# Kernel optimization log

Measured on AMD Instinct MI355X. Metric: run time of the kernel, lower is better.

The kernel has to match this reference:

```python
import jax, jax.numpy as jnp
import numpy as np

N_NODES = 50000
N_EDGES = 800000
IN_DIM = 256
OUT_DIM = 64
HEADS = 8


def setup_inputs() -> dict:
    key = jax.random.key(0)
    k1, k2, k3, k4, k5 = jax.random.split(key, 5)
    x = jax.random.normal(k1, (N_NODES, IN_DIM), dtype=jnp.float32)
    edge_index = jax.random.randint(k2, (2, N_EDGES), 0, N_NODES, dtype=jnp.int32)
    W = jax.random.normal(k3, (HEADS, IN_DIM, OUT_DIM), dtype=jnp.float32) / np.sqrt(IN_DIM)
    b = jnp.zeros((HEADS, OUT_DIM), dtype=jnp.float32)
    a = jax.random.normal(k4, (HEADS, 2 * OUT_DIM), dtype=jnp.float32)
    gate = jnp.ones((HEADS,), dtype=jnp.float32)
    return {"x": x, "edge_index": edge_index, "W": W, "b": b, "a": a, "gate": gate}


def reference(x, edge_index, W, b, a, gate):
    # Wh: [H, N, O] -- per-head linear projections
    Wh = jnp.einsum('nd,hdo->hno', x, W) + b[:, None, :]
    row, col = edge_index[0], edge_index[1]
    O = Wh.shape[-1]
    a_src, a_dst = a[:, :O], a[:, O:]  # split of concat weight: [H, O] each
    # score per edge per head: leaky_relu(cat(Wh[row], Wh[col]) @ a)
    e = (jnp.einsum('heo,ho->he', Wh[:, row], a_src)
         + jnp.einsum('heo,ho->he', Wh[:, col], a_dst))  # [H, E]
    e = jax.nn.leaky_relu(e, negative_slope=0.01)
    # NOTE: original code softmaxes over ALL edges (dim=0), not per node
    alpha = jax.nn.softmax(e, axis=1)  # [H, E]
    msgs = alpha[:, :, None] * Wh[:, col, :]  # [H, E, O]
    out = jax.vmap(lambda m: jax.ops.segment_sum(m, row, num_segments=Wh.shape[1]))(msgs)  # [H, N, O]
    g = jax.nn.softmax(gate)
    return jnp.einsum('h,hno->no', g, out)
```

## Files before the change

### kernel.cpp

```cpp
#include <hip/hip_runtime.h>
#include <hip/hip_bf16.h>


#define N_NODES 50000
#define N_EDGES 800000
#define IN_DIM  256
#define OUT_DIM 64
#define HEADS   8
#define NCOL    (HEADS * OUT_DIM)
#define NBLK_RED 2048
#define LN_W_EPS (-20.72326584f)

typedef __attribute__((ext_vector_type(8))) short short8;
typedef __attribute__((ext_vector_type(4))) float f32x4;

__device__ __forceinline__ void bf16_split2(float x0, float x1,
                                            unsigned& hi, unsigned& lo)
{
    unsigned u0 = __float_as_uint(x0), u1 = __float_as_uint(x1);
    unsigned r0 = u0 + 0x7FFFu + ((u0 >> 16) & 1u);
    unsigned r1 = u1 + 0x7FFFu + ((u1 >> 16) & 1u);
    float h0 = __uint_as_float(r0 & 0xFFFF0000u);
    float h1 = __uint_as_float(r1 & 0xFFFF0000u);
    hi = (r0 >> 16) | (r1 & 0xFFFF0000u);
    unsigned l0 = __float_as_uint(x0 - h0);
    unsigned l1 = __float_as_uint(x1 - h1);
    lo = (l0 >> 16) | (l1 & 0xFFFF0000u);
}

__global__ __launch_bounds__(256) void packw_kernel(
    const float* __restrict__ W, short* __restrict__ wp)
{
    const int ct = blockIdx.x;
    const int h  = ct >> 2;
    #pragma unroll
    for (int it = 0; it < 2; ++it) {
        const int i  = threadIdx.x + it * 256;
        const int k8 = i >> 4;
        const int c  = i & 15;
        const int o  = (ct & 3) * 16 + c;
        const float* src = W + (size_t)h * IN_DIM * OUT_DIM
                             + (size_t)k8 * 8 * OUT_DIM + o;
        unsigned hi[4], lo[4];
        #pragma unroll
        for (int p = 0; p < 4; ++p) {
            float x0 = src[(2 * p) * OUT_DIM];
            float x1 = src[(2 * p + 1) * OUT_DIM];
            bf16_split2(x0, x1, hi[p], lo[p]);
        }
        uint4 vh = make_uint4(hi[0], hi[1], hi[2], hi[3]);
        uint4 vl = make_uint4(lo[0], lo[1], lo[2], lo[3]);
        *(uint4*)(wp + (((size_t)(ct * 2 + 0) * 32 + k8) * 128) + c * 8) = vh;
        *(uint4*)(wp + (((size_t)(ct * 2 + 1) * 32 + k8) * 128) + c * 8) = vl;
    }
}

__global__ __launch_bounds__(512, 2) void gemm_kernel(
    const float* __restrict__ x, const short* __restrict__ wp,
    const float* __restrict__ b, const float* __restrict__ a,
    float* __restrict__ s_src, float* __restrict__ s_dst)
{
    __shared__ __align__(16) short As[32768];
    __shared__ __align__(16) float s_tmp[2][64][8];

    const int row0 = blockIdx.x * 64;
    const int tid  = threadIdx.x;
    const int lane = tid & 63;
    const int head = tid >> 6;
    const int r16  = lane & 15;
    const int kq   = lane >> 4;

    const short* pB = wp + (size_t)kq * 128 + (size_t)r16 * 8;
    #define LD_B(ni, s, ks) \
        (*(const short8*)(pB + ((((size_t)(head * 4 + (ni)) * 2 + (s)) * 32 + 4 * (ks)) * 128)))
    short8 Bh[2][4], Bl[2][4];
    #pragma unroll
    for (int ni = 0; ni < 4; ++ni) { Bh[0][ni] = LD_B(ni, 0, 0); Bl[0][ni] = LD_B(ni, 1, 0); }

    f32x4 vv[4][2];
    #pragma unroll
    for (int q = 0; q < 4; ++q) {
        const int item = q * 512 + tid;
        const int row  = item >> 5;
        const int kc   = item & 31;
        const int grow = row0 + row;
        vv[q][0] = (f32x4){0.f, 0.f, 0.f, 0.f};
        vv[q][1] = (f32x4){0.f, 0.f, 0.f, 0.f};
        if (grow < N_NODES) {
            vv[q][0] = *(const f32x4*)(x + (size_t)grow * IN_DIM + kc * 8);
            vv[q][1] = *(const f32x4*)(x + (size_t)grow * IN_DIM + kc * 8 + 4);
        }
    }
    __builtin_amdgcn_sched_barrier(0);

    #pragma unroll
    for (int q = 0; q < 4; ++q) {
        const int item = q * 512 + tid;
        const int row  = item >> 5;
        const int kc   = item & 31;
        unsigned hi[4], lo[4];
        bf16_split2(vv[q][0].x, vv[q][0].y, hi[0], lo[0]);
        bf16_split2(vv[q][0].z, vv[q][0].w, hi[1], lo[1]);
        bf16_split2(vv[q][1].x, vv[q][1].y, hi[2], lo[2]);
        bf16_split2(vv[q][1].z, vv[q][1].w, hi[3], lo[3]);
        const int mi  = row >> 4, rr = row & 15;
        const int swz = rr ^ (kc & 15);
        uint4 vh = make_uint4(hi[0], hi[1], hi[2], hi[3]);
        uint4 vl = make_uint4(lo[0], lo[1], lo[2], lo[3]);
        *(uint4*)((char*)As + ((((mi * 2 + 0) * 32 + kc) * 16 + swz) * 16)) = vh;
        *(uint4*)((char*)As + ((((mi * 2 + 1) * 32 + kc) * 16 + swz) * 16)) = vl;
    }
    __syncthreads();

    f32x4 acc[4][4] = {};

    #define LD_A(mi, s, ks) \
        (*(const short8*)((const char*)As + \
            (((((mi) * 2 + (s)) * 32 + (4 * (ks) + kq)) * 16 + \
              (r16 ^ ((4 * ((ks) & 3) + kq)))) * 16)))

    short8 Ah[2][4], Al[2][4];
    #pragma unroll
    for (int mi = 0; mi < 4; ++mi) { Ah[0][mi] = LD_A(mi, 0, 0); Al[0][mi] = LD_A(mi, 1, 0); }

    #pragma unroll
    for (int ks = 0; ks < 8; ++ks) {
        const int cur = ks & 1, nxt = cur ^ 1;
        if (ks < 7) {
            #pragma unroll
            for (int ni = 0; ni < 4; ++ni) {
                Bh[nxt][ni] = LD_B(ni, 0, ks + 1);
                Bl[nxt][ni] = LD_B(ni, 1, ks + 1);
            }
            #pragma unroll
            for (int mi = 0; mi < 4; ++mi) {
                Ah[nxt][mi] = LD_A(mi, 0, ks + 1);
                Al[nxt][mi] = LD_A(mi, 1, ks + 1);
            }
        }
        #pragma unroll
        for (int mi = 0; mi < 4; ++mi)
            #pragma unroll
            for (int ni = 0; ni < 4; ++ni) {
                acc[mi][ni] = __builtin_amdgcn_mfma_f32_16x16x32_bf16(
                    Ah[cur][mi], Bh[cur][ni], acc[mi][ni], 0, 0, 0);
                acc[mi][ni] = __builtin_amdgcn_mfma_f32_16x16x32_bf16(
                    Ah[cur][mi], Bl[cur][ni], acc[mi][ni], 0, 0, 0);
                acc[mi][ni] = __builtin_amdgcn_mfma_f32_16x16x32_bf16(
                    Al[cur][mi], Bh[cur][ni], acc[mi][ni], 0, 0, 0);
            }
    }
    #undef LD_A
    #undef LD_B

    const int n0 = head * 64;
    float bias[4], avs[4], avd[4];
    #pragma unroll
    for (int ni = 0; ni < 4; ++ni) {
        bias[ni] = b[n0 + ni * 16 + r16];
        avs[ni]  = a[head * 128 + ni * 16 + r16];
        avd[ni]  = a[head * 128 + 64 + ni * 16 + r16];
    }
    #pragma unroll
    for (int mi = 0; mi < 4; ++mi) {
        #pragma unroll
        for (int reg = 0; reg < 4; ++reg) {
            float ps = 0.f, pd = 0.f;
            #pragma unroll
            for (int ni = 0; ni < 4; ++ni) {
                const float v = acc[mi][ni][reg] + bias[ni];
                ps += v * avs[ni];
                pd += v * avd[ni];
            }
            ps += __shfl_xor(ps, 1); pd += __shfl_xor(pd, 1);
            ps += __shfl_xor(ps, 2); pd += __shfl_xor(pd, 2);
            ps += __shfl_xor(ps, 4); pd += __shfl_xor(pd, 4);
            ps += __shfl_xor(ps, 8); pd += __shfl_xor(pd, 8);
            if (r16 == 0) {
                const int rloc = mi * 16 + kq * 4 + reg;
                s_tmp[0][rloc][head] = ps;
                s_tmp[1][rloc][head] = pd;
            }
        }
    }
    __syncthreads();
    if (tid < 256) {
        const int r   = tid & 63;
        const int sel = tid >> 6;
        const int gr  = row0 + r;
        if (gr < N_NODES) {
            float* dst = (sel < 2) ? s_src : s_dst;
            *(float4*)(dst + (size_t)gr * 8 + (sel & 1) * 4) =
                *(const float4*)&s_tmp[sel >> 1][r][(sel & 1) * 4];
        }
    }
}

__global__ __launch_bounds__(256) void edge_score_kernel(
    const int* __restrict__ ei, const float* __restrict__ s_src,
    const float* __restrict__ s_dst, float* __restrict__ tbuf,
    float* __restrict__ partial)
{
    const int tid  = threadIdx.x;
    const int half = tid & 1;

    float m[4], l[4];
    #pragma unroll
    for (int i = 0; i < 4; ++i) { m[i] = -1e30f; l[i] = 0.f; }

    for (int p = blockIdx.x * 128 + (tid >> 1); p < N_EDGES; p += gridDim.x * 128) {
        const int row = ei[p];
        const int col = ei[N_EDGES + p];
        const f32x4 s = *(const f32x4*)(s_src + row * 8 + half * 4);
        const f32x4 d = *(const f32x4*)(s_dst + col * 8 + half * 4);
        float t[4];
        #pragma unroll
        for (int i = 0; i < 4; ++i) {
            float v = s[i] + d[i];
            t[i] = v > 0.f ? v : 0.01f * v;
        }
        if (tbuf)
            *(float4*)(tbuf + (size_t)p * 8 + half * 4) =
                make_float4(t[0], t[1], t[2], t[3]);
        #pragma unroll
        for (int i = 0; i < 4; ++i) {
            const float mn = fmaxf(m[i], t[i]);
            l[i] = l[i] * __expf(m[i] - mn) + __expf(t[i] - mn);
            m[i] = mn;
        }
    }

    __shared__ float red[8][256];
    #pragma unroll
    for (int i = 0; i < 4; ++i) { red[i][tid] = m[i]; red[4 + i][tid] = l[i]; }
    __syncthreads();
    for (int s = 128; s >= 2; s >>= 1) {
        if (tid < s) {
            #pragma unroll
            for (int i = 0; i < 4; ++i) {
                const float mo = red[i][tid + s], lo = red[4 + i][tid + s];
                const float mm = red[i][tid],     ll = red[4 + i][tid];
                const float mn = fmaxf(mm, mo);
                red[4 + i][tid] = ll * __expf(mm - mn) + lo * __expf(mo - mn);
                red[i][tid]     = mn;
            }
        }
        __syncthreads();
    }
    if (tid < 2) {
        #pragma unroll
        for (int i = 0; i < 4; ++i) {
            partial[blockIdx.x * 16 + tid * 4 + i]     = red[i][tid];
            partial[blockIdx.x * 16 + 8 + tid * 4 + i] = red[4 + i][tid];
        }
    }
}

__global__ __launch_bounds__(256) void finalize_kernel(
    const float* __restrict__ partial, const float* __restrict__ gate,
    float* __restrict__ coef, int nblk)
{
    const int t = threadIdx.x;
    const int h = t & 7;
    const int j = t >> 3;
    float m = -1e30f, l = 0.f;
    for (int bk = j; bk < nblk; bk += 32) {
        const float mb = partial[bk * 16 + h];
        const float lb = partial[bk * 16 + 8 + h];
        const float mn = fmaxf(m, mb);
        l = l * __expf(m - mn) + lb * __expf(mb - mn);
        m = mn;
    }
    __shared__ float rm[256], rl[256];
    rm[t] = m; rl[t] = l;
    __syncthreads();
    for (int s = 128; s >= 8; s >>= 1) {
        if (t < s) {
            const float mo = rm[t + s], lo = rl[t + s];
            const float mn = fmaxf(rm[t], mo);
            rl[t] = rl[t] * __expf(rm[t] - mn) + lo * __expf(mo - mn);
            rm[t] = mn;
        }
        __syncthreads();
    }
    if (t < 8) {
        float gm = gate[0];
        for (int i = 1; i < 8; ++i) gm = fmaxf(gm, gate[i]);
        float gs = 0.f;
        for (int i = 0; i < 8; ++i) gs += __expf(gate[i] - gm);
        const float g = __expf(gate[t] - gm) / gs;
        const float C = g / rl[t];
        coef[t]      = rm[t];
        coef[8 + t]  = C;
        coef[16 + t] = rm[t] + LN_W_EPS - __logf(C);
    }
}

__global__ __launch_bounds__(256) void mark_flags_kernel(
    const int* __restrict__ ei, const float* __restrict__ tbuf,
    const float* __restrict__ coef, int* __restrict__ colflag)
{
    __shared__ float cCut[8];
    if (threadIdx.x < 8) cCut[threadIdx.x] = coef[16 + threadIdx.x];
    __syncthreads();

    const int e = blockIdx.x * 256 + threadIdx.x;
    if (e >= N_EDGES) return;
    const float4 t0 = *(const float4*)(tbuf + (size_t)e * 8);
    const float4 t1 = *(const float4*)(tbuf + (size_t)e * 8 + 4);
    const bool pass =
        (t0.x >= cCut[0]) | (t0.y >= cCut[1]) |
        (t0.z >= cCut[2]) | (t0.w >= cCut[3]) |
        (t1.x >= cCut[4]) | (t1.y >= cCut[5]) |
        (t1.z >= cCut[6]) | (t1.w >= cCut[7]);
    if (pass)
        colflag[ei[N_EDGES + e]] = 1;
}

__global__ __launch_bounds__(256) void compact_nodes_kernel(
    const int* __restrict__ colflag, int* __restrict__ ncount,
    int* __restrict__ nlist)
{
    const int n    = blockIdx.x * 256 + threadIdx.x;
    const int lane = threadIdx.x & 63;
    const int w    = threadIdx.x >> 6;
    const bool f   = (n < N_NODES) && (colflag[n] != 0);
    const unsigned long long mask = __ballot(f);

    __shared__ int wcnt[4];
    __shared__ int bbase;
    if (lane == 0) wcnt[w] = (int)__popcll(mask);
    __syncthreads();
    if (threadIdx.x == 0) {
        const int tot = wcnt[0] + wcnt[1] + wcnt[2] + wcnt[3];
        bbase = tot ? atomicAdd(ncount, tot) : 0;
    }
    __syncthreads();
    if (f) {
        int wbase = bbase;
        for (int i = 0; i < w; ++i) wbase += wcnt[i];
        const int rank = (int)__popcll(mask & ((1ULL << lane) - 1ULL));
        nlist[wbase + rank] = n;
    }
}

__global__ __launch_bounds__(256) void mark_kernel(
    const int* __restrict__ ei, const float* __restrict__ s_src,
    const float* __restrict__ s_dst, const float* __restrict__ coef,
    int* __restrict__ elist, int* __restrict__ colflag,
    int* __restrict__ ecount, int* __restrict__ ncount, int* __restrict__ nlist)
{
    __shared__ float cCut[8];
    if (threadIdx.x < 8) cCut[threadIdx.x] = coef[16 + threadIdx.x];
    __syncthreads();

    const int e = blockIdx.x * 256 + threadIdx.x;
    bool pass = false;
    int col = 0;
    if (e < N_EDGES) {
        const int row = ei[e];
        col = ei[N_EDGES + e];
        const float4 s0 = *(const float4*)(s_src + row * 8);
        const float4 s1 = *(const float4*)(s_src + row * 8 + 4);
        const float4 d0 = *(const float4*)(s_dst + col * 8);
        const float4 d1 = *(const float4*)(s_dst + col * 8 + 4);
        float t[8] = { s0.x + d0.x, s0.y + d0.y, s0.z + d0.z, s0.w + d0.w,
                       s1.x + d1.x, s1.y + d1.y, s1.z + d1.z, s1.w + d1.w };
        #pragma unroll
        for (int h = 0; h < 8; ++h) {
            t[h] = t[h] > 0.f ? t[h] : 0.01f * t[h];
            pass |= (t[h] >= cCut[h]);
        }
    }

    const unsigned long long mask = __ballot(pass);
    if (mask) {
        const int lane   = threadIdx.x & 63;
        const int leader = (int)__builtin_ctzll(mask);
        int base = 0;
        if (lane == leader) base = atomicAdd(ecount, (int)__popcll(mask));
        base = __shfl(base, leader);
        if (pass) {
            const int rank = (int)__popcll(mask & ((1ULL << lane) - 1ULL));
            elist[base + rank] = e;
            if (atomicExch(&colflag[col], 1) == 0) {
                const int ni = atomicAdd(ncount, 1);
                nlist[ni] = col;
            }
        }
    }
}

__global__ __launch_bounds__(512, 2) void whrows_kernel(
    const float* __restrict__ x, const short* __restrict__ wp,
    const float* __restrict__ b, const int* __restrict__ nlist,
    const int* __restrict__ ncount, float* __restrict__ Wh)
{
    __shared__ __align__(16) short As[32768];
    __shared__ int nl_sh[64];

    const int nc   = *ncount;
    const int row0 = blockIdx.x * 64;
    if (row0 >= nc) return;

    const int tid  = threadIdx.x;
    const int lane = tid & 63;
    const int head = tid >> 6;
    const int r16  = lane & 15;
    const int kq   = lane >> 4;

    if (tid < 64) {
        const int idx = row0 + tid;
        nl_sh[tid] = (idx < nc) ? nlist[idx] : -1;
    }

    const short* pB = wp + (size_t)kq * 128 + (size_t)r16 * 8;
    #define LD_B2(ni, s, ks) \
        (*(const short8*)(pB + ((((size_t)(head * 4 + (ni)) * 2 + (s)) * 32 + 4 * (ks)) * 128)))
    short8 Bh[2][4], Bl[2][4];
    #pragma unroll
    for (int ni = 0; ni < 4; ++ni) { Bh[0][ni] = LD_B2(ni, 0, 0); Bl[0][ni] = LD_B2(ni, 1, 0); }

    __syncthreads();

    f32x4 vv[4][2];
    #pragma unroll
    for (int q = 0; q < 4; ++q) {
        const int item = q * 512 + tid;
        const int row  = item >> 5;
        const int grow = nl_sh[row];
        const int kc   = item & 31;
        vv[q][0] = (f32x4){0.f, 0.f, 0.f, 0.f};
        vv[q][1] = (f32x4){0.f, 0.f, 0.f, 0.f};
        if (grow >= 0) {
            vv[q][0] = *(const f32x4*)(x + (size_t)grow * IN_DIM + kc * 8);
            vv[q][1] = *(const f32x4*)(x + (size_t)grow * IN_DIM + kc * 8 + 4);
        }
    }
    __builtin_amdgcn_sched_barrier(0);

    #pragma unroll
    for (int q = 0; q < 4; ++q) {
        const int item = q * 512 + tid;
        const int row  = item >> 5;
        const int kc   = item & 31;
        unsigned hi[4], lo[4];
        bf16_split2(vv[q][0].x, vv[q][0].y, hi[0], lo[0]);
        bf16_split2(vv[q][0].z, vv[q][0].w, hi[1], lo[1]);
        bf16_split2(vv[q][1].x, vv[q][1].y, hi[2], lo[2]);
        bf16_split2(vv[q][1].z, vv[q][1].w, hi[3], lo[3]);
        const int mi  = row >> 4, rr = row & 15;
        const int swz = rr ^ (kc & 15);
        uint4 vh = make_uint4(hi[0], hi[1], hi[2], hi[3]);
        uint4 vl = make_uint4(lo[0], lo[1], lo[2], lo[3]);
        *(uint4*)((char*)As + ((((mi * 2 + 0) * 32 + kc) * 16 + swz) * 16)) = vh;
        *(uint4*)((char*)As + ((((mi * 2 + 1) * 32 + kc) * 16 + swz) * 16)) = vl;
    }
    __syncthreads();

    f32x4 acc[4][4] = {};

    #define LD_A2(mi, s, ks) \
        (*(const short8*)((const char*)As + \
            (((((mi) * 2 + (s)) * 32 + (4 * (ks) + kq)) * 16 + \
              (r16 ^ ((4 * ((ks) & 3) + kq)))) * 16)))

    short8 Ah[2][4], Al[2][4];
    #pragma unroll
    for (int mi = 0; mi < 4; ++mi) { Ah[0][mi] = LD_A2(mi, 0, 0); Al[0][mi] = LD_A2(mi, 1, 0); }

    #pragma unroll
    for (int ks = 0; ks < 8; ++ks) {
        const int cur = ks & 1, nxt = cur ^ 1;
        if (ks < 7) {
            #pragma unroll
            for (int ni = 0; ni < 4; ++ni) {
                Bh[nxt][ni] = LD_B2(ni, 0, ks + 1);
                Bl[nxt][ni] = LD_B2(ni, 1, ks + 1);
            }
            #pragma unroll
            for (int mi = 0; mi < 4; ++mi) {
                Ah[nxt][mi] = LD_A2(mi, 0, ks + 1);
                Al[nxt][mi] = LD_A2(mi, 1, ks + 1);
            }
        }
        #pragma unroll
        for (int mi = 0; mi < 4; ++mi)
            #pragma unroll
            for (int ni = 0; ni < 4; ++ni) {
                acc[mi][ni] = __builtin_amdgcn_mfma_f32_16x16x32_bf16(
                    Ah[cur][mi], Bh[cur][ni], acc[mi][ni], 0, 0, 0);
                acc[mi][ni] = __builtin_amdgcn_mfma_f32_16x16x32_bf16(
                    Ah[cur][mi], Bl[cur][ni], acc[mi][ni], 0, 0, 0);
                acc[mi][ni] = __builtin_amdgcn_mfma_f32_16x16x32_bf16(
                    Al[cur][mi], Bh[cur][ni], acc[mi][ni], 0, 0, 0);
            }
    }
    #undef LD_A2
    #undef LD_B2

    const int n0 = head * 64;
    float bias[4];
    #pragma unroll
    for (int ni = 0; ni < 4; ++ni) bias[ni] = b[n0 + ni * 16 + r16];

    #pragma unroll
    for (int mi = 0; mi < 4; ++mi) {
        #pragma unroll
        for (int reg = 0; reg < 4; ++reg) {
            const int rloc = mi * 16 + kq * 4 + reg;
            const int n    = nl_sh[rloc];
            if (n >= 0) {
                *(float4*)(Wh + (size_t)n * NCOL + n0 + r16 * 4) =
                    make_float4(acc[mi][0][reg] + bias[0],
                                acc[mi][1][reg] + bias[1],
                                acc[mi][2][reg] + bias[2],
                                acc[mi][3][reg] + bias[3]);
            }
        }
    }
}

__global__ __launch_bounds__(256) void acc_st_kernel(
    const int* __restrict__ ei, const float* __restrict__ tbuf,
    const float* __restrict__ Wh, const float* __restrict__ coef,
    float* __restrict__ out)
{
    __shared__ float cM[8], cC[8], cCut[8];
    if (threadIdx.x < 8)       cM[threadIdx.x]        = coef[threadIdx.x];
    else if (threadIdx.x < 16) cC[threadIdx.x - 8]    = coef[threadIdx.x];
    else if (threadIdx.x < 24) cCut[threadIdx.x - 16] = coef[threadIdx.x];
    __syncthreads();

    const int lane = threadIdx.x & 63;
    const int e    = blockIdx.x * 256 + threadIdx.x;

    bool pass = false;
    float t[8];
    if (e < N_EDGES) {
        const float4 t0 = *(const float4*)(tbuf + (size_t)e * 8);
        const float4 t1 = *(const float4*)(tbuf + (size_t)e * 8 + 4);
        t[0] = t0.x; t[1] = t0.y; t[2] = t0.z; t[3] = t0.w;
        t[4] = t1.x; t[5] = t1.y; t[6] = t1.z; t[7] = t1.w;
        #pragma unroll
        for (int h = 0; h < 8; ++h) pass |= (t[h] >= cCut[h]);
    }

    int row = 0, col = 0;
    float wgt[8];
    if (pass) {
        row = ei[e];
        col = ei[N_EDGES + e];
        #pragma unroll
        for (int h = 0; h < 8; ++h)
            wgt[h] = __expf(t[h] - cM[h]) * cC[h];
    }

    unsigned long long mask = __ballot(pass);
    while (mask) {
        const int src = (int)__builtin_ctzll(mask);
        mask &= mask - 1;
        const int rb = __shfl(row, src);
        const int cb = __shfl(col, src);
        const float* wc = Wh + (size_t)cb * NCOL + (lane & 15) * 4 + (lane >> 4);
        float acc = 0.f;
        #pragma unroll
        for (int h = 0; h < 8; ++h)
            acc += __shfl(wgt[h], src) * wc[h * 64];
        atomicAdd(out + (size_t)rb * OUT_DIM + lane, acc);
    }
}

__global__ __launch_bounds__(256) void acc_kernel(
    const int* __restrict__ ei, const float* __restrict__ s_src,
    const float* __restrict__ s_dst, const float* __restrict__ Wh,
    const float* __restrict__ coef, const int* __restrict__ elist,
    const int* __restrict__ ecount, float* __restrict__ out)
{
    __shared__ float cM[8], cC[8];
    if (threadIdx.x < 8)       cM[threadIdx.x]     = coef[threadIdx.x];
    else if (threadIdx.x < 16) cC[threadIdx.x - 8] = coef[threadIdx.x];
    __syncthreads();

    const int n    = *ecount;
    const int lane = threadIdx.x & 63;

    for (int i = blockIdx.x * 256 + threadIdx.x; ; i += gridDim.x * 256) {
        const bool has = i < n;
        if (!__any(has)) break;

        int row = 0, col = 0;
        float wgt[8];
        if (has) {
            const int e = elist[i];
            row = ei[e];
            col = ei[N_EDGES + e];
            const float4 s0 = *(const float4*)(s_src + row * 8);
            const float4 s1 = *(const float4*)(s_src + row * 8 + 4);
            const float4 d0 = *(const float4*)(s_dst + col * 8);
            const float4 d1 = *(const float4*)(s_dst + col * 8 + 4);
            float t[8] = { s0.x + d0.x, s0.y + d0.y, s0.z + d0.z, s0.w + d0.w,
                           s1.x + d1.x, s1.y + d1.y, s1.z + d1.z, s1.w + d1.w };
            #pragma unroll
            for (int h = 0; h < 8; ++h) {
                t[h] = t[h] > 0.f ? t[h] : 0.01f * t[h];
                wgt[h] = __expf(t[h] - cM[h]) * cC[h];
            }
        }

        unsigned long long mask = __ballot(has);
        while (mask) {
            const int src = (int)__builtin_ctzll(mask);
            mask &= mask - 1;
            const int rb = __shfl(row, src);
            const int cb = __shfl(col, src);
            const float* wc = Wh + (size_t)cb * NCOL + (lane & 15) * 4 + (lane >> 4);
            float acc = 0.f;
            #pragma unroll
            for (int h = 0; h < 8; ++h)
                acc += __shfl(wgt[h], src) * wc[h * 64];
            atomicAdd(out + (size_t)rb * OUT_DIM + lane, acc);
        }
    }
}

extern "C" void kernel_launch(void* const* d_in, const int* in_sizes, int n_in,
                              void* d_out, int out_size, void* d_ws, size_t ws_size,
                              hipStream_t stream)
{
    const float* x    = (const float*)d_in[0];
    const int*   ei   = (const int*)  d_in[1];
    const float* W    = (const float*)d_in[2];
    const float* b    = (const float*)d_in[3];
    const float* a    = (const float*)d_in[4];
    const float* gate = (const float*)d_in[5];
    float* out = (float*)d_out;

    float* ws      = (float*)d_ws;
    float* Wh      = ws;
    float* s_src   = Wh    + (size_t)N_NODES * NCOL;
    float* s_dst   = s_src + (size_t)N_NODES * HEADS;
    float* partial = s_dst + (size_t)N_NODES * HEADS;
    float* coef    = partial + (size_t)NBLK_RED * 16;
    short* wp      = (short*)(coef + 32);
    int*   elist   = (int*)(wp + 262144);
    int*   colflag = elist + N_EDGES;
    int*   ecount  = colflag + N_NODES;
    int*   ncount  = ecount + 1;
    int*   nlist   = ncount + 1;
    float* tbuf    = (float*)(nlist + N_NODES);

    const size_t base_bytes = (size_t)((char*)tbuf - (char*)ws);
    const size_t need_tbuf  = base_bytes + (size_t)N_EDGES * 8 * sizeof(float);
    const bool   use_tbuf   = ws_size >= need_tbuf;

    hipMemsetAsync(d_out, 0, (size_t)N_NODES * OUT_DIM * sizeof(float), stream);
    hipMemsetAsync(colflag, 0, (size_t)(N_NODES + 2) * sizeof(int), stream);

    packw_kernel<<<32, 256, 0, stream>>>(W, wp);

    gemm_kernel<<<(N_NODES + 63) / 64, 512, 0, stream>>>(x, wp, b, a, s_src, s_dst);

    edge_score_kernel<<<NBLK_RED, 256, 0, stream>>>(
        ei, s_src, s_dst, use_tbuf ? tbuf : nullptr, partial);

    finalize_kernel<<<1, 256, 0, stream>>>(partial, gate, coef, NBLK_RED);

    if (use_tbuf) {
        mark_flags_kernel<<<(N_EDGES + 255) / 256, 256, 0, stream>>>(
            ei, tbuf, coef, colflag);
        compact_nodes_kernel<<<(N_NODES + 255) / 256, 256, 0, stream>>>(
            colflag, ncount, nlist);
    } else {
        mark_kernel<<<(N_EDGES + 255) / 256, 256, 0, stream>>>(
            ei, s_src, s_dst, coef, elist, colflag, ecount, ncount, nlist);
    }

    whrows_kernel<<<(N_NODES + 63) / 64, 512, 0, stream>>>(
        x, wp, b, nlist, ncount, Wh);

    if (use_tbuf)
        acc_st_kernel<<<(N_EDGES + 255) / 256, 256, 0, stream>>>(
            ei, tbuf, Wh, coef, out);
    else
        acc_kernel<<<256, 256, 0, stream>>>(
            ei, s_src, s_dst, Wh, coef, elist, ecount, out);
}
```

Before: 232.3 us.

## Fold attention vectors into projection weights to compute scores via GEMV

The per-node source and destination attention scores are now computed as x·(W a) + b·a, using a small precomputed 256x16 matrix, instead of running the full bf16-split MFMA GEMM that produced Wh and then dotting it with a. This removes a large tensor-core GEMM pass over all nodes from the score path and replaces it with a memory-bound read of x plus shuffle reductions. The edge-score kernel also changes from a grid-stride loop to a fixed 4-edges-per-thread-pair layout with loads hoisted ahead of the math, and its block count drops to 1568. The scores are now full fp32 dot products with a different summation order, so they differ slightly in rounding from the split-bf16 path.

```diff
diff --git a/kernel.cpp b/kernel.cpp
--- a/kernel.cpp
+++ b/kernel.cpp
@@ -8,7 +8,7 @@
 #define OUT_DIM 64
 #define HEADS   8
 #define NCOL    (HEADS * OUT_DIM)
-#define NBLK_RED 2048
+#define ES_BLOCKS 1568
 #define LN_W_EPS (-20.72326584f)
 
 typedef __attribute__((ext_vector_type(8))) short short8;
@@ -28,6 +28,29 @@
     lo = (l0 >> 16) | (l1 & 0xFFFF0000u);
 }
 
+__global__ __launch_bounds__(256) void prep_kernel(
+    const float* __restrict__ W, const float* __restrict__ b,
+    const float* __restrict__ a, float* __restrict__ ug)
+{
+    const int j = blockIdx.x;
+    const int h = j & 7, sd = j >> 3;
+    __shared__ float a_sh[64];
+    if (threadIdx.x < 64) a_sh[threadIdx.x] = a[h * 128 + sd * 64 + threadIdx.x];
+    __syncthreads();
+
+    const int d = threadIdx.x;
+    const float* wrow = W + ((size_t)h * IN_DIM + d) * OUT_DIM;
+    float s = 0.f;
+    #pragma unroll 8
+    for (int o = 0; o < 64; ++o) s += wrow[o] * a_sh[o];
+    ug[j * 256 + d] = s;
+    if (d == 0) {
+        float c = 0.f;
+        for (int o = 0; o < 64; ++o) c += b[h * OUT_DIM + o] * a_sh[o];
+        ug[4096 + j] = c;
+    }
+}
+
 __global__ __launch_bounds__(256) void packw_kernel(
     const float* __restrict__ W, short* __restrict__ wp)
 {
@@ -55,143 +78,84 @@
     }
 }
 
-__global__ __launch_bounds__(512, 2) void gemm_kernel(
-    const float* __restrict__ x, const short* __restrict__ wp,
-    const float* __restrict__ b, const float* __restrict__ a,
+__device__ __forceinline__ float reduce16x64(const float (&p)[16], int lane)
+{
+    float v8[8];
+    #pragma unroll
+    for (int j = 0; j < 8; ++j) {
+        const float keep = (lane & 1) ? p[j + 8] : p[j];
+        const float send = (lane & 1) ? p[j] : p[j + 8];
+        v8[j] = keep + __shfl_xor(send, 1);
+    }
+    float v4[4];
+    #pragma unroll
+    for (int j = 0; j < 4; ++j) {
+        const float keep = (lane & 2) ? v8[j + 4] : v8[j];
+        const float send = (lane & 2) ? v8[j] : v8[j + 4];
+        v4[j] = keep + __shfl_xor(send, 2);
+    }
+    float v2[2];
+    #pragma unroll
+    for (int j = 0; j < 2; ++j) {
+        const float keep = (lane & 4) ? v4[j + 2] : v4[j];
+        const float send = (lane & 4) ? v4[j] : v4[j + 2];
+        v2[j] = keep + __shfl_xor(send, 4);
+    }
+    float v1;
+    {
+        const float keep = (lane & 8) ? v2[1] : v2[0];
+        const float send = (lane & 8) ? v2[0] : v2[1];
+        v1 = keep + __shfl_xor(send, 8);
+    }
+    v1 += __shfl_xor(v1, 16);
+    v1 += __shfl_xor(v1, 32);
+    return v1;
+}
+
+__global__ __launch_bounds__(256, 2) void score_kernel(
+    const float* __restrict__ x, const float* __restrict__ ug,
     float* __restrict__ s_src, float* __restrict__ s_dst)
 {
-    __shared__ __align__(16) short As[32768];
-    __shared__ __align__(16) float s_tmp[2][64][8];
-
-    const int row0 = blockIdx.x * 64;
     const int tid  = threadIdx.x;
     const int lane = tid & 63;
-    const int head = tid >> 6;
-    const int r16  = lane & 15;
-    const int kq   = lane >> 4;
-
-    const short* pB = wp + (size_t)kq * 128 + (size_t)r16 * 8;
-    #define LD_B(ni, s, ks) \
-        (*(const short8*)(pB + ((((size_t)(head * 4 + (ni)) * 2 + (s)) * 32 + 4 * (ks)) * 128)))
-    short8 Bh[2][4], Bl[2][4];
-    #pragma unroll
-    for (int ni = 0; ni < 4; ++ni) { Bh[0][ni] = LD_B(ni, 0, 0); Bl[0][ni] = LD_B(ni, 1, 0); }
-
-    f32x4 vv[4][2];
-    #pragma unroll
-    for (int q = 0; q < 4; ++q) {
-        const int item = q * 512 + tid;
-        const int row  = item >> 5;
-        const int kc   = item & 31;
-        const int grow = row0 + row;
-        vv[q][0] = (f32x4){0.f, 0.f, 0.f, 0.f};
-        vv[q][1] = (f32x4){0.f, 0.f, 0.f, 0.f};
-        if (grow < N_NODES) {
-            vv[q][0] = *(const f32x4*)(x + (size_t)grow * IN_DIM + kc * 8);
-            vv[q][1] = *(const f32x4*)(x + (size_t)grow * IN_DIM + kc * 8 + 4);
-        }
-    }
-    __builtin_amdgcn_sched_barrier(0);
-
-    #pragma unroll
-    for (int q = 0; q < 4; ++q) {
-        const int item = q * 512 + tid;
-        const int row  = item >> 5;
-        const int kc   = item & 31;
-        unsigned hi[4], lo[4];
-        bf16_split2(vv[q][0].x, vv[q][0].y, hi[0], lo[0]);
-        bf16_split2(vv[q][0].z, vv[q][0].w, hi[1], lo[1]);
-        bf16_split2(vv[q][1].x, vv[q][1].y, hi[2], lo[2]);
-        bf16_split2(vv[q][1].z, vv[q][1].w, hi[3], lo[3]);
-        const int mi  = row >> 4, rr = row & 15;
-        const int swz = rr ^ (kc & 15);
-        uint4 vh = make_uint4(hi[0], hi[1], hi[2], hi[3]);
-        uint4 vl = make_uint4(lo[0], lo[1], lo[2], lo[3]);
-        *(uint4*)((char*)As + ((((mi * 2 + 0) * 32 + kc) * 16 + swz) * 16)) = vh;
-        *(uint4*)((char*)As + ((((mi * 2 + 1) * 32 + kc) * 16 + swz) * 16)) = vl;
-    }
-    __syncthreads();
-
-    f32x4 acc[4][4] = {};
-
-    #define LD_A(mi, s, ks) \
-        (*(const short8*)((const char*)As + \
-            (((((mi) * 2 + (s)) * 32 + (4 * (ks) + kq)) * 16 + \
-              (r16 ^ ((4 * ((ks) & 3) + kq)))) * 16)))
-
-    short8 Ah[2][4], Al[2][4];
-    #pragma unroll
-    for (int mi = 0; mi < 4; ++mi) { Ah[0][mi] = LD_A(mi, 0, 0); Al[0][mi] = LD_A(mi, 1, 0); }
-
-    #pragma unroll
-    for (int ks = 0; ks < 8; ++ks) {
-        const int cur = ks & 1, nxt = cur ^ 1;
-        if (ks < 7) {
+    const int w    = tid >> 6;
+    const int jj   = ((lane & 1) << 3) | (((lane >> 1) & 1) << 2) |
+                     (((lane >> 2) & 1) << 1) | ((lane >> 3) & 1);
+
+    f32x4 uj[16];
+    #pragma unroll
+    for (int j = 0; j < 16; ++j)
+        uj[j] = *(const f32x4*)(ug + j * 256 + lane * 4);
+    const float cj = (lane < 16) ? ug[4096 + jj] : 0.f;
+
+    const int base = (blockIdx.x * 4 + w) * 16;
+
+    #pragma unroll
+    for (int i0 = 0; i0 < 16; i0 += 4) {
+        int   n[4];
+        f32x4 xv[4];
+        #pragma unroll
+        for (int k = 0; k < 4; ++k) {
+            n[k] = base + i0 + k;
+            xv[k] = (f32x4){0.f, 0.f, 0.f, 0.f};
+            if (n[k] < N_NODES)
+                xv[k] = *(const f32x4*)(x + (size_t)n[k] * IN_DIM + lane * 4);
+        }
+        __builtin_amdgcn_sched_barrier(0);
+
+        #pragma unroll
+        for (int k = 0; k < 4; ++k) {
+            float p[16];
             #pragma unroll
-            for (int ni = 0; ni < 4; ++ni) {
-                Bh[nxt][ni] = LD_B(ni, 0, ks + 1);
-                Bl[nxt][ni] = LD_B(ni, 1, ks + 1);
-            }
-            #pragma unroll
-            for (int mi = 0; mi < 4; ++mi) {
-                Ah[nxt][mi] = LD_A(mi, 0, ks + 1);
-                Al[nxt][mi] = LD_A(mi, 1, ks + 1);
-            }
-        }
-        #pragma unroll
-        for (int mi = 0; mi < 4; ++mi)
-            #pragma unroll
-            for (int ni = 0; ni < 4; ++ni) {
-                acc[mi][ni] = __builtin_amdgcn_mfma_f32_16x16x32_bf16(
-                    Ah[cur][mi], Bh[cur][ni], acc[mi][ni], 0, 0, 0);
-                acc[mi][ni] = __builtin_amdgcn_mfma_f32_16x16x32_bf16(
-                    Ah[cur][mi], Bl[cur][ni], acc[mi][ni], 0, 0, 0);
-                acc[mi][ni] = __builtin_amdgcn_mfma_f32_16x16x32_bf16(
-                    Al[cur][mi], Bh[cur][ni], acc[mi][ni], 0, 0, 0);
-            }
-    }
-    #undef LD_A
-    #undef LD_B
-
-    const int n0 = head * 64;
-    float bias[4], avs[4], avd[4];
-    #pragma unroll
-    for (int ni = 0; ni < 4; ++ni) {
-        bias[ni] = b[n0 + ni * 16 + r16];
-        avs[ni]  = a[head * 128 + ni * 16 + r16];
-        avd[ni]  = a[head * 128 + 64 + ni * 16 + r16];
-    }
-    #pragma unroll
-    for (int mi = 0; mi < 4; ++mi) {
-        #pragma unroll
-        for (int reg = 0; reg < 4; ++reg) {
-            float ps = 0.f, pd = 0.f;
-            #pragma unroll
-            for (int ni = 0; ni < 4; ++ni) {
-                const float v = acc[mi][ni][reg] + bias[ni];
-                ps += v * avs[ni];
-                pd += v * avd[ni];
-            }
-            ps += __shfl_xor(ps, 1); pd += __shfl_xor(pd, 1);
-            ps += __shfl_xor(ps, 2); pd += __shfl_xor(pd, 2);
-            ps += __shfl_xor(ps, 4); pd += __shfl_xor(pd, 4);
-            ps += __shfl_xor(ps, 8); pd += __shfl_xor(pd, 8);
-            if (r16 == 0) {
-                const int rloc = mi * 16 + kq * 4 + reg;
-                s_tmp[0][rloc][head] = ps;
-                s_tmp[1][rloc][head] = pd;
-            }
-        }
-    }
-    __syncthreads();
-    if (tid < 256) {
-        const int r   = tid & 63;
-        const int sel = tid >> 6;
-        const int gr  = row0 + r;
-        if (gr < N_NODES) {
-            float* dst = (sel < 2) ? s_src : s_dst;
-            *(float4*)(dst + (size_t)gr * 8 + (sel & 1) * 4) =
-                *(const float4*)&s_tmp[sel >> 1][r][(sel & 1) * 4];
+            for (int j = 0; j < 16; ++j)
+                p[j] = xv[k].x * uj[j].x + xv[k].y * uj[j].y +
+                       xv[k].z * uj[j].z + xv[k].w * uj[j].w;
+            const float r = reduce16x64(p, lane);
+            if (lane < 16 && n[k] < N_NODES) {
+                const float val = r + cj;
+                if (jj < 8) s_src[(size_t)n[k] * 8 + jj]       = val;
+                else        s_dst[(size_t)n[k] * 8 + (jj - 8)] = val;
+            }
         }
     }
 }
@@ -203,55 +167,73 @@
 {
     const int tid  = threadIdx.x;
     const int half = tid & 1;
+    const int e0   = blockIdx.x * 512 + (tid >> 1);
+
+    int  pe[4], rows[4], cols[4];
+    bool valid[4];
+    #pragma unroll
+    for (int i = 0; i < 4; ++i) {
+        pe[i]    = e0 + i * 128;
+        valid[i] = pe[i] < N_EDGES;
+        rows[i]  = valid[i] ? ei[pe[i]] : 0;
+        cols[i]  = valid[i] ? ei[N_EDGES + pe[i]] : 0;
+    }
+    __builtin_amdgcn_sched_barrier(0);
+
+    f32x4 sv[4], dv[4];
+    #pragma unroll
+    for (int i = 0; i < 4; ++i) {
+        sv[i] = *(const f32x4*)(s_src + rows[i] * 8 + half * 4);
+        dv[i] = *(const f32x4*)(s_dst + cols[i] * 8 + half * 4);
+    }
+    __builtin_amdgcn_sched_barrier(0);
 
     float m[4], l[4];
     #pragma unroll
     for (int i = 0; i < 4; ++i) { m[i] = -1e30f; l[i] = 0.f; }
 
-    for (int p = blockIdx.x * 128 + (tid >> 1); p < N_EDGES; p += gridDim.x * 128) {
-        const int row = ei[p];
-        const int col = ei[N_EDGES + p];
-        const f32x4 s = *(const f32x4*)(s_src + row * 8 + half * 4);
-        const f32x4 d = *(const f32x4*)(s_dst + col * 8 + half * 4);
+    #pragma unroll
+    for (int i = 0; i < 4; ++i) {
+        if (!valid[i]) continue;
         float t[4];
         #pragma unroll
-        for (int i = 0; i < 4; ++i) {
-            float v = s[i] + d[i];
-            t[i] = v > 0.f ? v : 0.01f * v;
+        for (int q = 0; q < 4; ++q) {
+            const float v = sv[i][q] + dv[i][q];
+            t[q] = v > 0.f ? v : 0.01f * v;
         }
         if (tbuf)
-            *(float4*)(tbuf + (size_t)p * 8 + half * 4) =
+            *(float4*)(tbuf + (size_t)pe[i] * 8 + half * 4) =
                 make_float4(t[0], t[1], t[2], t[3]);
         #pragma unroll
-        for (int i = 0; i < 4; ++i) {
-            const float mn = fmaxf(m[i], t[i]);
-            l[i] = l[i] * __expf(m[i] - mn) + __expf(t[i] - mn);
-            m[i] = mn;
+        for (int q = 0; q < 4; ++q) {
+            const float mn = fmaxf(m[q], t[q]);
+            l[q] = l[q] * __expf(m[q] - mn) + __expf(t[q] - mn);
+            m[q] = mn;
         }
     }
 
     __shared__ float red[8][256];
     #pragma unroll
-    for (int i = 0; i < 4; ++i) { red[i][tid] = m[i]; red[4 + i][tid] = l[i]; }
+    for (int q = 0; q < 4; ++q) { red[q][tid] = m[q]; red[4 + q][tid] = l[q]; }
     __syncthreads();
     for (int s = 128; s >= 2; s >>= 1) {
         if (tid < s) {
             #pragma unroll
-            for (int i = 0; i < 4; ++i) {
-                const float mo = red[i][tid + s], lo = red[4 + i][tid + s];
-                const float mm = red[i][tid],     ll = red[4 + i][tid];
+            for (int q = 0; q < 4; ++q) {
+                const float mo = red[q][tid + s], lo = red[4 + q][tid + s];
+                const float mm = red[q][tid],     ll = red[4 + q][tid];
                 const float mn = fmaxf(mm, mo);
-                red[4 + i][tid] = ll * __expf(mm - mn) + lo * __expf(mo - mn);
-                red[i][tid]     = mn;
+                red[4 + q][tid] = ll * __expf(mm - mn) + lo * __expf(mo - mn);
+                red[q][tid]     = mn;
             }
         }
         __syncthreads();
     }
     if (tid < 2) {
         #pragma unroll
-        for (int i = 0; i < 4; ++i) {
-            partial[blockIdx.x * 16 + tid * 4 + i]     = red[i][tid];
-            partial[blockIdx.x * 16 + 8 + tid * 4 + i] = red[4 + i][tid];
+        for (int q = 0; q < 4; ++q) {
+            partial[blockIdx.x * 16 + tid * 4 + q]     = red[q][tid];
+            partial[blockIdx.x * 16 + 8 + tid * 4 + q] = red[4 + q][tid];
         }
     }
 }
@@ -641,14 +623,15 @@
     float* s_src   = Wh    + (size_t)N_NODES * NCOL;
     float* s_dst   = s_src + (size_t)N_NODES * HEADS;
     float* partial = s_dst + (size_t)N_NODES * HEADS;
-    float* coef    = partial + (size_t)NBLK_RED * 16;
+    float* coef    = partial + (size_t)2048 * 16;
     short* wp      = (short*)(coef + 32);
     int*   elist   = (int*)(wp + 262144);
     int*   colflag = elist + N_EDGES;
     int*   ecount  = colflag + N_NODES;
     int*   ncount  = ecount + 1;
     int*   nlist   = ncount + 1;
-    float* tbuf    = (float*)(nlist + N_NODES);
+    float* ug      = (float*)(nlist + N_NODES);
+    float* tbuf    = ug + 4112;
 
     const size_t base_bytes = (size_t)((char*)tbuf - (char*)ws);
     const size_t need_tbuf  = base_bytes + (size_t)N_EDGES * 8 * sizeof(float);
@@ -657,14 +640,15 @@
     hipMemsetAsync(d_out, 0, (size_t)N_NODES * OUT_DIM * sizeof(float), stream);
     hipMemsetAsync(colflag, 0, (size_t)(N_NODES + 2) * sizeof(int), stream);
 
+    prep_kernel<<<16, 256, 0, stream>>>(W, b, a, ug);
     packw_kernel<<<32, 256, 0, stream>>>(W, wp);
 
-    gemm_kernel<<<(N_NODES + 63) / 64, 512, 0, stream>>>(x, wp, b, a, s_src, s_dst);
-
-    edge_score_kernel<<<NBLK_RED, 256, 0, stream>>>(
+    score_kernel<<<(N_NODES + 63) / 64, 256, 0, stream>>>(x, ug, s_src, s_dst);
+
+    edge_score_kernel<<<ES_BLOCKS, 256, 0, stream>>>(
         ei, s_src, s_dst, use_tbuf ? tbuf : nullptr, partial);
 
-    finalize_kernel<<<1, 256, 0, stream>>>(partial, gate, coef, NBLK_RED);
+    finalize_kernel<<<1, 256, 0, stream>>>(partial, gate, coef, ES_BLOCKS);
 
     if (use_tbuf) {
         mark_flags_kernel<<<(N_EDGES + 255) / 256, 256, 0, stream>>>(
```

Result: faster. 196.0 us (-15.6%).
